# Kernel tuning notes

Measured on AMD Instinct MI355X. Metric: run time of the kernel, lower is better.

Reference implementation:

```python
import jax, jax.numpy as jnp
import numpy as np

B, S, V = 2, 4096, 50265
L, DM, DFF = 2, 768, 3072
H, D, W = 12, 64, 256  # heads, head_dim, one-sided window (attention_window=512)
NEG = -1e9


def _ln(x, s, b, eps=1e-5):
    m = x.mean(-1, keepdims=True)
    v = ((x - m) ** 2).mean(-1, keepdims=True)
    return (x - m) * jax.lax.rsqrt(v + eps) * s + b


def _heads(y):  # [B,S,DM] -> [B,H,S,D]
    return y.reshape(B, S, H, D).transpose(0, 2, 1, 3)


def _longformer_layer(x, am, p):
    nb = S // W  # number of query blocks
    scale = 1.0 / jnp.sqrt(jnp.asarray(D, x.dtype))
    q = _heads(x @ p['Wq'] + p['bq']) * scale
    k = _heads(x @ p['Wk'] + p['bk'])
    v = _heads(x @ p['Wv'] + p['bv'])
    # overlapping key blocks: block n covers padded positions [n*W, n*W+3W)
    idx = jnp.arange(nb)[:, None] * W + jnp.arange(3 * W)[None, :]  # [nb,3W]
    kp = jnp.pad(k, ((0, 0), (0, 0), (W, W), (0, 0)))
    vp = jnp.pad(v, ((0, 0), (0, 0), (W, W), (0, 0)))
    kb = kp[:, :, idx]  # [B,H,nb,3W,D]
    vb = vp[:, :, idx]
    qb = q.reshape(B, H, nb, W, D)
    scores = jnp.einsum('bhnqd,bhnkd->bhnqk', qb, kb)  # [B,H,nb,W,3W]
    # band mask: query i attends keys within +-W
    qi = jnp.arange(W)[:, None]
    kj = jnp.arange(3 * W)[None, :]
    band = (kj >= qi) & (kj <= qi + 2 * W)  # [W,3W]
    kpos = idx - W  # global key positions, [nb,3W]
    valid = (kpos >= 0) & (kpos < S) & (kpos != 0)  # exclude global tok 0 from band
    amk = jnp.pad(am, ((0, 0), (W, W)))[:, idx] > 0  # [B,nb,3W]
    mask = band[None, None, None] & valid[None, None, :, None, :] & amk[:, None, :, None, :]
    scores = jnp.where(mask, scores, NEG).reshape(B, H, S, 3 * W)
    # global-key column: every query attends token 0 (regular K/V)
    sg = jnp.einsum('bhsd,bhd->bhs', q, k[:, :, 0])
    sg = jnp.where(am[:, None, 0:1] > 0, sg, NEG)
    attn = jax.nn.softmax(jnp.concatenate([scores, sg[..., None]], -1), axis=-1)
    a_band = attn[..., :3 * W].reshape(B, H, nb, W, 3 * W)
    out = jnp.einsum('bhnqk,bhnkd->bhnqd', a_band, vb).reshape(B, H, S, D)
    out = out + attn[..., 3 * W][..., None] * v[:, :, 0][:, :, None, :]
    # global query row (token 0): full attention with dedicated global projections
    qg = ((x[:, 0] @ p['Wqg'] + p['bqg']).reshape(B, H, D)) * scale
    kg = _heads(x @ p['Wkg'] + p['bkg'])
    vg = _heads(x @ p['Wvg'] + p['bvg'])
    sgl = jnp.einsum('bhd,bhsd->bhs', qg, kg)
    sgl = jnp.where(am[:, None, :] > 0, sgl, NEG)
    og = jnp.einsum('bhs,bhsd->bhd', jax.nn.softmax(sgl, axis=-1), vg)
    out = out.at[:, :, 0, :].set(og)
    attn_out = out.transpose(0, 2, 1, 3).reshape(B, S, DM) @ p['Wo'] + p['bo']
    x = _ln(x + attn_out, p['ln1_s'], p['ln1_b'])
    h = jax.nn.gelu(x @ p['W1'] + p['b1']) @ p['W2'] + p['b2']
    return _ln(x + h, p['ln2_s'], p['ln2_b'])


def setup_inputs() -> dict:
    key = jax.random.key(0)
    ks = iter(jax.random.split(key, 40))
    f = lambda *s: jax.random.normal(next(ks), s, jnp.float32) * 0.02
    inp = {
        'input_ids': jax.random.randint(next(ks), (B, S), 0, V),
        'attention_mask': jnp.ones((B, S), jnp.int32),
        'word_emb': f(V, DM), 'pos_emb': f(S, DM),
        'ln_e_s': jnp.ones((DM,)), 'ln_e_b': jnp.zeros((DM,)),
        'Wq': f(L, DM, DM), 'bq': jnp.zeros((L, DM)),
        'Wk': f(L, DM, DM), 'bk': jnp.zeros((L, DM)),
        'Wv': f(L, DM, DM), 'bv': jnp.zeros((L, DM)),
        'Wqg': f(L, DM, DM), 'bqg': jnp.zeros((L, DM)),
        'Wkg': f(L, DM, DM), 'bkg': jnp.zeros((L, DM)),
        'Wvg': f(L, DM, DM), 'bvg': jnp.zeros((L, DM)),
        'Wo': f(L, DM, DM), 'bo': jnp.zeros((L, DM)),
        'ln1_s': jnp.ones((L, DM)), 'ln1_b': jnp.zeros((L, DM)),
        'W1': f(L, DM, DFF), 'b1': jnp.zeros((L, DFF)),
        'W2': f(L, DFF, DM), 'b2': jnp.zeros((L, DM)),
        'ln2_s': jnp.ones((L, DM)), 'ln2_b': jnp.zeros((L, DM)),
        'Wcls': f(DM, 2), 'bcls': jnp.zeros((2,)),
    }
    return inp


def reference(input_ids, attention_mask, word_emb, pos_emb, ln_e_s, ln_e_b,
              Wq, bq, Wk, bk, Wv, bv, Wqg, bqg, Wkg, bkg, Wvg, bvg, Wo, bo,
              ln1_s, ln1_b, W1, b1, W2, b2, ln2_s, ln2_b, Wcls, bcls):
    x = word_emb[input_ids] + pos_emb[None]
    x = _ln(x, ln_e_s, ln_e_b)
    for l in range(L):
        p = dict(Wq=Wq[l], bq=bq[l], Wk=Wk[l], bk=bk[l], Wv=Wv[l], bv=bv[l],
                 Wqg=Wqg[l], bqg=bqg[l], Wkg=Wkg[l], bkg=bkg[l], Wvg=Wvg[l], bvg=bvg[l],
                 Wo=Wo[l], bo=bo[l], ln1_s=ln1_s[l], ln1_b=ln1_b[l],
                 W1=W1[l], b1=b1[l], W2=W2[l], b2=b2[l], ln2_s=ln2_s[l], ln2_b=ln2_b[l])
        x = _longformer_layer(x, attention_mask, p)
    return x[:, 0] @ Wcls + bcls  # logits [B, num_labels]
```

## Files before the change

### kernel.cpp

```cpp
#include <hip/hip_runtime.h>
#include <hip/hip_bf16.h>

#define B_   2
#define S_   4096
#define DM_  768
#define H_   12
#define D_   64
#define W_   256
#define NB_  16
#define DFF_ 3072
#define L_   2
#define QS_  3840
#define NEG_ (-1.0e9f)
#define GC_  16

typedef long long ll;
typedef unsigned short u16;
typedef unsigned int   u32;

typedef __attribute__((ext_vector_type(8))) short bfrag;
typedef __attribute__((ext_vector_type(4))) float ffrag;
typedef __attribute__((address_space(1))) unsigned gu32;
typedef __attribute__((address_space(3))) unsigned lu32;

__device__ __forceinline__ float b2f(u16 u){ union{u32 i; float f;} x; x.i = ((u32)u)<<16; return x.f; }
__device__ __forceinline__ u16 f2b(float f){
  __hip_bfloat16 h = __float2bfloat16(f);
  union{__hip_bfloat16 h; u16 u;} x; x.h = h; return x.u;
}
__device__ __forceinline__ void unp8(uint4 u, float* f){
  union{u32 i; float v;} a;
  a.i = u.x<<16; f[0]=a.v; a.i = u.x&0xffff0000u; f[1]=a.v;
  a.i = u.y<<16; f[2]=a.v; a.i = u.y&0xffff0000u; f[3]=a.v;
  a.i = u.z<<16; f[4]=a.v; a.i = u.z&0xffff0000u; f[5]=a.v;
  a.i = u.w<<16; f[6]=a.v; a.i = u.w&0xffff0000u; f[7]=a.v;
}
__device__ __forceinline__ void gld16(const void* g, void* l){
  __builtin_amdgcn_global_load_lds((gu32*)g, (lu32*)l, 16, 0, 0);
}
__device__ __forceinline__ float bsum256(float v, float* s4){
  #pragma unroll
  for(int o=32;o>0;o>>=1) v += __shfl_down(v,o,64);
  int w = threadIdx.x>>6;
  __syncthreads();
  if((threadIdx.x&63)==0) s4[w]=v;
  __syncthreads();
  return s4[0]+s4[1]+s4[2]+s4[3];
}
__device__ __forceinline__ float bmax256(float v, float* s4){
  #pragma unroll
  for(int o=32;o>0;o>>=1) v = fmaxf(v,__shfl_down(v,o,64));
  int w = threadIdx.x>>6;
  __syncthreads();
  if((threadIdx.x&63)==0) s4[w]=v;
  __syncthreads();
  return fmaxf(fmaxf(s4[0],s4[1]),fmaxf(s4[2],s4[3]));
}
__device__ __forceinline__ float gelu_f(float x){
  return 0.5f*x*(1.0f+tanhf(0.7978845608028654f*(x+0.044715f*x*x*x)));
}

__global__ void k_detect(const void* les, int* flag){
  unsigned u = *(const unsigned*)les;
  *flag = (u == 0x3F803F80u) ? 1 : 0;
}

__global__ void k_cvt(const void* __restrict__ src, ll soff, float* __restrict__ dst, int n, const int* flag){
  int f = *flag;
  int i = blockIdx.x*256 + threadIdx.x;
  int st = gridDim.x*256;
  if(f){
    const u16* s = (const u16*)src + soff;
    for(; i<n; i+=st) dst[i] = b2f(s[i]);
  } else {
    const float* s = (const float*)src + soff;
    for(; i<n; i+=st) dst[i] = s[i];
  }
}

struct CvtArgs { const void* src[32]; float* dst[32]; int soff[32]; int n[32]; };
__global__ void k_cvts(CvtArgs a, const int* __restrict__ flag){
  int seg = blockIdx.y;
  int i = blockIdx.x*256 + threadIdx.x;
  if(i >= a.n[seg]) return;
  int f = *flag;
  float v = f ? b2f(((const u16*)a.src[seg])[a.soff[seg]+i])
              : ((const float*)a.src[seg])[a.soff[seg]+i];
  a.dst[seg][i] = v;
}

__global__ __launch_bounds__(256) void k_tw(const void* __restrict__ src, ll soff, u16* __restrict__ dst,
    int R, int C, const int* __restrict__ flag){
  __shared__ float tile[32][33];
  int f = *flag;
  int tx = threadIdx.x & 31, ty = threadIdx.x >> 5;
  int c = blockIdx.x*32 + tx;
  #pragma unroll
  for(int i=0;i<4;i++){
    int r = blockIdx.y*32 + ty + i*8;
    float v;
    if(f) v = b2f(((const u16*)src)[soff + (ll)r*C + c]);
    else  v = ((const float*)src)[soff + (ll)r*C + c];
    tile[ty + i*8][tx] = v;
  }
  __syncthreads();
  #pragma unroll
  for(int i=0;i<4;i++){
    int orow = blockIdx.x*32 + ty + i*8;
    int oc   = blockIdx.y*32 + tx;
    dst[(ll)orow*R + oc] = f2b(tile[tx][ty + i*8]);
  }
}

struct TwArgs { const void* src[14]; ll soff[14]; u16* dst[14]; };
__global__ __launch_bounds__(256) void k_tws(TwArgs a, const int* __restrict__ flag){
  __shared__ float tile[32][33];
  int z = blockIdx.z;
  const void* src = a.src[z]; ll soff = a.soff[z]; u16* dst = a.dst[z];
  int f = *flag;
  int tx = threadIdx.x & 31, ty = threadIdx.x >> 5;
  int c = blockIdx.x*32 + tx;
  #pragma unroll
  for(int i=0;i<4;i++){
    int r = blockIdx.y*32 + ty + i*8;
    float v;
    if(f) v = b2f(((const u16*)src)[soff + (ll)r*DM_ + c]);
    else  v = ((const float*)src)[soff + (ll)r*DM_ + c];
    tile[ty + i*8][tx] = v;
  }
  __syncthreads();
  #pragma unroll
  for(int i=0;i<4;i++){
    int orow = blockIdx.x*32 + ty + i*8;
    int oc   = blockIdx.y*32 + tx;
    dst[(ll)orow*DM_ + oc] = f2b(tile[tx][ty + i*8]);
  }
}

__global__ __launch_bounds__(256) void k_embed(const int* __restrict__ ids, const void* __restrict__ wemb,
    const float* __restrict__ pos, const float* __restrict__ es, const float* __restrict__ eb,
    float* __restrict__ x, u16* __restrict__ xb, const int* flag){
  __shared__ float s4[4];
  int tok = blockIdx.x;
  int s = tok & (S_-1);
  int t = threadIdx.x;
  int id = ids[tok];
  int f = *flag;
  float v[3];
  #pragma unroll
  for(int j=0;j<3;j++){
    int i = t + j*256;
    float we = f ? b2f(((const u16*)wemb)[(ll)id*DM_ + i])
                 : ((const float*)wemb)[(ll)id*DM_ + i];
    v[j] = we + pos[s*DM_ + i];
  }
  float mean = bsum256(v[0]+v[1]+v[2], s4) * (1.0f/DM_);
  float d0=v[0]-mean, d1=v[1]-mean, d2=v[2]-mean;
  float var = bsum256(d0*d0+d1*d1+d2*d2, s4) * (1.0f/DM_);
  float r = rsqrtf(var + 1e-5f);
  #pragma unroll
  for(int j=0;j<3;j++){
    int i = t + j*256;
    float o = (v[j]-mean)*r*es[i] + eb[i];
    x[(ll)tok*DM_ + i] = o;
    xb[(ll)tok*DM_ + i] = f2b(o);
  }
}

__global__ __launch_bounds__(256) void k_rln(float* __restrict__ x, const float* __restrict__ add,
    const float* __restrict__ sc, const float* __restrict__ bi, u16* __restrict__ xb){
  __shared__ float s4[4];
  int tok = blockIdx.x;
  int t = threadIdx.x;
  float v[3];
  #pragma unroll
  for(int j=0;j<3;j++){
    int i = t + j*256;
    v[j] = x[(ll)tok*DM_+i] + add[(ll)tok*DM_+i];
  }
  float mean = bsum256(v[0]+v[1]+v[2], s4) * (1.0f/DM_);
  float d0=v[0]-mean, d1=v[1]-mean, d2=v[2]-mean;
  float var = bsum256(d0*d0+d1*d1+d2*d2, s4) * (1.0f/DM_);
  float r = rsqrtf(var + 1e-5f);
  #pragma unroll
  for(int j=0;j<3;j++){
    int i = t + j*256;
    float o = (v[j]-mean)*r*sc[i] + bi[i];
    x[(ll)tok*DM_+i] = o;
    xb[(ll)tok*DM_+i] = f2b(o);
  }
}

template<int MODE>
__global__ __launch_bounds__(256) void k_mm(const u16* __restrict__ A, const u16* __restrict__ Bt,
    const float* __restrict__ bias, void* __restrict__ Cout, int M, int N, int K){
  __shared__ __align__(16) u16 As[128*32];
  __shared__ __align__(16) u16 Bs[128*32];
  int tid = threadIdx.x, wave = tid>>6, lane = tid&63;
  int m0 = blockIdx.y*128, n0 = blockIdx.x*128;
  int wm = (wave>>1)*64, wn = (wave&1)*64;
  ffrag acc[4][4];
  #pragma unroll
  for(int i=0;i<4;i++)
    #pragma unroll
    for(int j=0;j<4;j++) acc[i][j] = (ffrag){0.f,0.f,0.f,0.f};
  int lrow = lane>>2, lseg = (lane&3)*8;
  const u16* Ap0 = A  + (ll)(m0 + wave*32 + lrow)*K + lseg;
  const u16* Bp0 = Bt + (ll)(n0 + wave*32 + lrow)*K + lseg;
  u16* AsW0 = As + (wave*2+0)*512;
  u16* AsW1 = As + (wave*2+1)*512;
  u16* BsW0 = Bs + (wave*2+0)*512;
  u16* BsW1 = Bs + (wave*2+1)*512;
  int lane15 = lane&15, quad = lane>>4;
  const u16* ArA = As + (wm + lane15)*32 + quad*8;
  const u16* BrB = Bs + (wn + lane15)*32 + quad*8;
  for(int k0=0; k0<K; k0+=32){
    __syncthreads();
    gld16(Ap0 + k0,             AsW0);
    gld16(Ap0 + k0 + (ll)16*K,  AsW1);
    gld16(Bp0 + k0,             BsW0);
    gld16(Bp0 + k0 + (ll)16*K,  BsW1);
    __syncthreads();
    bfrag af[4], bf[4];
    #pragma unroll
    for(int i=0;i<4;i++) af[i] = *(const bfrag*)(ArA + i*512);
    #pragma unroll
    for(int i=0;i<4;i++) bf[i] = *(const bfrag*)(BrB + i*512);
    #pragma unroll
    for(int i=0;i<4;i++)
      #pragma unroll
      for(int j=0;j<4;j++)
        acc[i][j] = __builtin_amdgcn_mfma_f32_16x16x32_bf16(af[i], bf[j], acc[i][j], 0, 0, 0);
  }
  #pragma unroll
  for(int mi=0;mi<4;mi++){
    #pragma unroll
    for(int ni=0;ni<4;ni++){
      int col = n0 + wn + ni*16 + lane15;
      float bv = bias[col];
      #pragma unroll
      for(int r=0;r<4;r++){
        int row = m0 + wm + mi*16 + quad*4 + r;
        float c = acc[mi][ni][r] + bv;
        if(MODE==2) c = gelu_f(c);
        if(MODE==1) ((float*)Cout)[(ll)row*N + col] = c;
        else        ((u16*)Cout)[(ll)row*N + col] = f2b(c);
      }
    }
  }
}

__global__ __launch_bounds__(256) void k_qg(const float* __restrict__ x, const u16* __restrict__ Wt,
    const float* __restrict__ bg, float* __restrict__ qg){
  int b = blockIdx.y;
  int nn = blockIdx.x*256 + threadIdx.x;
  __shared__ float xs[DM_];
  int t = threadIdx.x;
  #pragma unroll
  for(int j=0;j<3;j++) xs[t + j*256] = x[(ll)(b*S_)*DM_ + t + j*256];
  __syncthreads();
  const uint4* wr = (const uint4*)(Wt + (ll)nn*DM_);
  float acc = bg[nn];
  #pragma unroll 4
  for(int g=0; g<96; g++){
    float tf[8]; unp8(wr[g], tf);
    #pragma unroll
    for(int e=0;e<8;e++) acc = fmaf(xs[g*8+e], tf[e], acc);
  }
  qg[b*DM_ + nn] = acc;
}

__global__ __launch_bounds__(256) void k_band(const u16* __restrict__ qb, const u16* __restrict__ kb,
    const u16* __restrict__ vb, const int* __restrict__ am, u16* __restrict__ aout){
  int n = blockIdx.x, h = blockIdx.y, b = blockIdx.z;
  int tid = threadIdx.x;
  int wave = tid>>6, lane = tid&63, lane15 = lane&15, quad = lane>>4;
  int wq = wave*64;
  __shared__ __align__(16) u16 Ks[32*72];
  __shared__ __align__(16) u16 Vt[64*40];
  __shared__ __align__(16) u16 Ps[4][64*40];
  __shared__ float k0f[64];
  __shared__ float v0f[64];
  __shared__ float cok[32];
  const int kbase = n*W_ - W_;
  const int am0 = am[b*S_];
  bfrag aq[4][2];
  {
    const u16* qbase = qb + ((ll)(b*S_ + n*W_ + wq + lane15))*QS_ + h*64 + quad*8;
    #pragma unroll
    for(int mi=0;mi<4;mi++)
      #pragma unroll
      for(int kc=0;kc<2;kc++)
        aq[mi][kc] = *(const bfrag*)(qbase + (ll)mi*16*QS_ + kc*32);
  }
  if(tid < 64){
    k0f[tid] = b2f(kb[(ll)(b*S_)*QS_ + h*64 + tid]);
    v0f[tid] = b2f(vb[(ll)(b*S_)*QS_ + h*64 + tid]);
  }
  ffrag ao[4][4];
  #pragma unroll
  for(int i=0;i<4;i++)
    #pragma unroll
    for(int j=0;j<4;j++) ao[i][j] = (ffrag){0.f,0.f,0.f,0.f};
  float ms[16], ls[16];
  #pragma unroll
  for(int i=0;i<16;i++){ ms[i] = -INFINITY; ls[i] = 0.f; }

  #pragma unroll 1
  for(int c=0;c<24;c++){
    __syncthreads();
    {
      int key = tid>>3, seg = tid&7;
      int kp = kbase + c*32 + key;
      uint4 kvec = make_uint4(0,0,0,0), vvec = make_uint4(0,0,0,0);
      if((unsigned)kp < (unsigned)S_){
        kvec = *(const uint4*)(kb + ((ll)(b*S_+kp))*QS_ + h*64 + seg*8);
        vvec = *(const uint4*)(vb + ((ll)(b*S_+kp))*QS_ + h*64 + seg*8);
      }
      *(uint4*)&Ks[key*72 + seg*8] = kvec;
      u16 vs[8]; *(uint4*)vs = vvec;
      #pragma unroll
      for(int i=0;i<8;i++) Vt[(seg*8+i)*40 + key] = vs[i];
      if(tid < 32){
        int kp2 = kbase + c*32 + tid;
        cok[tid] = ((kp2>=1) && (kp2<S_) && (am[b*S_+kp2]>0)) ? 0.f : NEG_;
      }
    }
    __syncthreads();
    ffrag as_[4][2];
    #pragma unroll
    for(int mi=0;mi<4;mi++)
      #pragma unroll
      for(int ni=0;ni<2;ni++) as_[mi][ni] = (ffrag){0.f,0.f,0.f,0.f};
    #pragma unroll
    for(int ni=0;ni<2;ni++){
      #pragma unroll
      for(int kc=0;kc<2;kc++){
        bfrag bk = *(const bfrag*)&Ks[(ni*16+lane15)*72 + kc*32 + quad*8];
        #pragma unroll
        for(int mi=0;mi<4;mi++)
          as_[mi][ni] = __builtin_amdgcn_mfma_f32_16x16x32_bf16(aq[mi][kc], bk, as_[mi][ni], 0, 0, 0);
      }
    }
    float c0 = cok[lane15], c1 = cok[16+lane15];
    int jg0 = c*32 + lane15, jg1 = jg0 + 16;
    #pragma unroll
    for(int mi=0;mi<4;mi++){
      #pragma unroll
      for(int reg=0;reg<4;reg++){
        int qloc = wq + mi*16 + quad*4 + reg;
        float s0 = ((unsigned)(jg0 - qloc) <= 512u) ? as_[mi][0][reg]*0.125f + c0 : NEG_;
        float s1 = ((unsigned)(jg1 - qloc) <= 512u) ? as_[mi][1][reg]*0.125f + c1 : NEG_;
        float cm = fmaxf(s0, s1);
        cm = fmaxf(cm, __shfl_xor(cm,1));
        cm = fmaxf(cm, __shfl_xor(cm,2));
        cm = fmaxf(cm, __shfl_xor(cm,4));
        cm = fmaxf(cm, __shfl_xor(cm,8));
        int si = mi*4 + reg;
        float mn = fmaxf(ms[si], cm);
        float al = __expf(ms[si] - mn);
        float p0 = __expf(s0 - mn), p1 = __expf(s1 - mn);
        float rs = p0 + p1;
        rs += __shfl_xor(rs,1); rs += __shfl_xor(rs,2);
        rs += __shfl_xor(rs,4); rs += __shfl_xor(rs,8);
        ls[si] = ls[si]*al + rs;
        ms[si] = mn;
        #pragma unroll
        for(int nt=0;nt<4;nt++) ao[mi][nt][reg] *= al;
        int prow = mi*16 + quad*4 + reg;
        Ps[wave][prow*40 + lane15]      = f2b(p0);
        Ps[wave][prow*40 + 16 + lane15] = f2b(p1);
      }
    }
    bfrag bv[4];
    #pragma unroll
    for(int nt=0;nt<4;nt++) bv[nt] = *(const bfrag*)&Vt[(nt*16+lane15)*40 + quad*8];
    #pragma unroll
    for(int mi=0;mi<4;mi++){
      bfrag ap = *(const bfrag*)&Ps[wave][(mi*16+lane15)*40 + quad*8];
      #pragma unroll
      for(int nt=0;nt<4;nt++)
        ao[mi][nt] = __builtin_amdgcn_mfma_f32_16x16x32_bf16(ap, bv[nt], ao[mi][nt], 0, 0, 0);
    }
  }
  float k0v[16];
  #pragma unroll
  for(int kc=0;kc<2;kc++)
    #pragma unroll
    for(int j=0;j<8;j++) k0v[kc*8+j] = k0f[kc*32 + quad*8 + j];
  float cokg = (am0>0) ? 0.f : NEG_;
  float sgm[4];
  #pragma unroll
  for(int mi=0;mi<4;mi++){
    float d = 0.f;
    #pragma unroll
    for(int kc=0;kc<2;kc++)
      #pragma unroll
      for(int j=0;j<8;j++)
        d = fmaf(b2f((u16)aq[mi][kc][j]), k0v[kc*8+j], d);
    d += __shfl_xor(d,16);
    d += __shfl_xor(d,32);
    sgm[mi] = d*0.125f + cokg;
  }
  float v0v[4];
  #pragma unroll
  for(int nt=0;nt<4;nt++) v0v[nt] = v0f[nt*16 + lane15];
  #pragma unroll
  for(int mi=0;mi<4;mi++){
    #pragma unroll
    for(int reg=0;reg<4;reg++){
      int si = mi*4 + reg;
      float sg = __shfl(sgm[mi], (quad<<4) + quad*4 + reg);
      float mn = fmaxf(ms[si], sg);
      float al = __expf(ms[si] - mn);
      float pg = __expf(sg - mn);
      float inv = 1.f / (ls[si]*al + pg);
      #pragma unroll
      for(int nt=0;nt<4;nt++)
        ao[mi][nt][reg] = (ao[mi][nt][reg]*al + pg*v0v[nt]) * inv;
    }
  }
  u16* obase = aout + ((ll)(b*S_ + n*W_ + wq + quad*4))*DM_ + h*64 + lane15;
  #pragma unroll
  for(int mi=0;mi<4;mi++)
    #pragma unroll
    for(int reg=0;reg<4;reg++)
      #pragma unroll
      for(int nt=0;nt<4;nt++)
        obase[(ll)(mi*16+reg)*DM_ + nt*16] = f2b(ao[mi][nt][reg]);
}

__global__ __launch_bounds__(256) void k_gattn1(const float* __restrict__ qg, const u16* __restrict__ kg,
    const u16* __restrict__ vg, const int* __restrict__ am, float* __restrict__ part){
  int ck = blockIdx.x, h = blockIdx.y, b = blockIdx.z;
  int t = threadIdx.x;
  __shared__ float s4[4];
  __shared__ float qgs[64];
  __shared__ float ps[256];
  __shared__ float obuf[4][64];
  if(t < 64) qgs[t] = qg[b*DM_ + h*64 + t];
  __syncthreads();
  int s = ck*256 + t;
  const uint4* kr = (const uint4*)(kg + (ll)(b*S_+s)*QS_ + h*64);
  float d = 0.f;
  #pragma unroll
  for(int g=0; g<8; g++){
    float tf[8]; unp8(kr[g], tf);
    #pragma unroll
    for(int e=0;e<8;e++) d = fmaf(qgs[g*8+e], tf[e], d);
  }
  float sc = (am[b*S_+s] > 0) ? d*0.125f : NEG_;
  float m_c = bmax256(sc, s4);
  float p = __expf(sc - m_c);
  float l_c = bsum256(p, s4);
  ps[t] = p;
  __syncthreads();
  int dd = t & 63, grp = t >> 6;
  float acc = 0.f;
  const u16* vbase = vg + (ll)(b*S_ + ck*256 + grp*64)*QS_ + h*64 + dd;
  #pragma unroll 8
  for(int j=0;j<64;j++)
    acc = fmaf(ps[grp*64+j], b2f(vbase[(ll)j*QS_]), acc);
  obuf[grp][dd] = acc;
  __syncthreads();
  if(t < 64){
    float o = obuf[0][t] + obuf[1][t] + obuf[2][t] + obuf[3][t];
    float* pp = part + ((ll)(b*H_+h)*GC_ + ck)*66;
    if(t == 0){ pp[0] = m_c; pp[1] = l_c; }
    pp[2+t] = o;
  }
}

__global__ void k_gattn2(const float* __restrict__ part, u16* __restrict__ aout){
  int h = blockIdx.x, b = blockIdx.y;
  int t = threadIdx.x;
  const float* pp = part + ((ll)(b*H_+h)*GC_)*66;
  float m = -INFINITY;
  #pragma unroll
  for(int c=0;c<GC_;c++) m = fmaxf(m, pp[c*66]);
  float l = 0.f, o = 0.f;
  #pragma unroll
  for(int c=0;c<GC_;c++){
    float w = __expf(pp[c*66] - m);
    l += pp[c*66+1]*w;
    o += pp[c*66+2+t]*w;
  }
  aout[(ll)(b*S_)*DM_ + h*64 + t] = f2b(o/l);
}

__global__ __launch_bounds__(256) void k_cls(const float* __restrict__ x, const float* __restrict__ Wc,
    const float* __restrict__ bc, void* out, const int* flag){
  __shared__ float s4[4];
  int t = threadIdx.x;
  float a00=0,a01=0,a10=0,a11=0;
  for(int k=t;k<DM_;k+=256){
    float w0 = Wc[k*2], w1 = Wc[k*2+1];
    float x0 = x[k];
    float x1 = x[(ll)S_*DM_ + k];
    a00 = fmaf(x0,w0,a00); a01 = fmaf(x0,w1,a01);
    a10 = fmaf(x1,w0,a10); a11 = fmaf(x1,w1,a11);
  }
  float r00 = bsum256(a00,s4);
  float r01 = bsum256(a01,s4);
  float r10 = bsum256(a10,s4);
  float r11 = bsum256(a11,s4);
  if(t==0){
    float o[4] = {r00+bc[0], r01+bc[1], r10+bc[0], r11+bc[1]};
    if(*flag){
      __hip_bfloat16* ob = (__hip_bfloat16*)out;
      for(int i=0;i<4;i++) ob[i] = __float2bfloat16(o[i]);
    } else {
      float* of = (float*)out;
      for(int i=0;i<4;i++) of[i] = o[i];
    }
  }
}

extern "C" void kernel_launch(void* const* d_in, const int* in_sizes, int n_in,
                              void* d_out, int out_size, void* d_ws, size_t ws_size,
                              hipStream_t stream){
  char* wsb = (char*)d_ws;
  size_t off = 0;
  auto alloc = [&](size_t bytes)->size_t{ off = (off + 255) & ~(size_t)255; size_t r = off; off += bytes; return r; };
  const size_t TOK = (size_t)B_*S_;
  size_t P_flag = alloc(16);
  size_t P_pos  = alloc((size_t)S_*DM_*4);
  size_t P_les  = alloc(DM_*4), P_leb = alloc(DM_*4);
  size_t P_bqkv = alloc((size_t)L_*QS_*4);
  size_t P_bqg  = alloc((size_t)L_*DM_*4);
  size_t P_bo   = alloc((size_t)L_*DM_*4);
  size_t P_b1   = alloc((size_t)L_*DFF_*4);
  size_t P_b2   = alloc((size_t)L_*DM_*4);
  size_t P_l1s  = alloc((size_t)L_*DM_*4), P_l1b = alloc((size_t)L_*DM_*4);
  size_t P_l2s  = alloc((size_t)L_*DM_*4), P_l2b = alloc((size_t)L_*DM_*4);
  size_t P_Wc   = alloc(DM_*2*4), P_bc = alloc(64);
  size_t P_qgb  = alloc((size_t)B_*DM_*4);
  size_t P_part = alloc((size_t)B_*H_*GC_*66*4);
  size_t P_Wqkvt= alloc((size_t)L_*QS_*DM_*2);
  size_t P_Wqgt = alloc((size_t)L_*DM_*DM_*2);
  size_t P_Wot  = alloc((size_t)L_*DM_*DM_*2);
  size_t P_W1t  = alloc((size_t)L_*DM_*DFF_*2);
  size_t P_W2t  = alloc((size_t)L_*DFF_*DM_*2);
  size_t P_x    = alloc(TOK*DM_*4);
  size_t P_tmp  = alloc(TOK*DM_*4);
  size_t P_xb   = alloc(TOK*DM_*2);
  size_t P_qkv  = alloc(TOK*QS_*2);
  size_t P_aout = alloc(TOK*DM_*2);
  size_t P_h    = alloc(TOK*DFF_*2);

  int* flag = (int*)(wsb + P_flag);
  #define FP(o) ((float*)(wsb + (o)))
  #define HP(o) ((u16*)(wsb + (o)))

  k_detect<<<1,1,0,stream>>>(d_in[4], flag);

  k_cvt<<<2048,256,0,stream>>>(d_in[3], 0, FP(P_pos), S_*DM_, flag);

  {
    CvtArgs ca{};
    int ns = 0;
    auto addcv = [&](int idx, size_t dstoff, int soff, int nelem){
      ca.src[ns] = d_in[idx]; ca.dst[ns] = FP(dstoff); ca.soff[ns] = soff; ca.n[ns] = nelem; ns++;
    };
    addcv(4, P_les, 0, DM_); addcv(5, P_leb, 0, DM_);
    addcv(28, P_Wc, 0, DM_*2); addcv(29, P_bc, 0, 2);
    const int bidx[5] = {7,9,11,15,17};
    for(int l=0;l<L_;l++){
      for(int s=0;s<5;s++) addcv(bidx[s], P_bqkv + ((size_t)l*QS_ + s*DM_)*4, l*DM_, DM_);
      addcv(13, P_bqg + (size_t)l*DM_*4,  l*DM_,  DM_);
      addcv(19, P_bo  + (size_t)l*DM_*4,  l*DM_,  DM_);
      addcv(23, P_b1  + (size_t)l*DFF_*4, l*DFF_, DFF_);
      addcv(25, P_b2  + (size_t)l*DM_*4,  l*DM_,  DM_);
      addcv(20, P_l1s + (size_t)l*DM_*4,  l*DM_,  DM_);
      addcv(21, P_l1b + (size_t)l*DM_*4,  l*DM_,  DM_);
      addcv(26, P_l2s + (size_t)l*DM_*4,  l*DM_,  DM_);
      addcv(27, P_l2b + (size_t)l*DM_*4,  l*DM_,  DM_);
    }
    for(int s2=ns; s2<32; s2++){ ca.src[s2]=d_in[4]; ca.dst[s2]=FP(P_les); ca.soff[s2]=0; ca.n[s2]=0; }
    k_cvts<<<dim3(12, ns),256,0,stream>>>(ca, flag);
  }

  {
    TwArgs ta{};
    int nt_ = 0;
    const int widx[5] = {6,8,10,14,16};
    for(int l=0;l<L_;l++){
      for(int s=0;s<5;s++){
        ta.src[nt_] = d_in[widx[s]]; ta.soff[nt_] = (ll)l*DM_*DM_;
        ta.dst[nt_] = HP(P_Wqkvt) + (size_t)l*QS_*DM_ + (size_t)s*DM_*DM_; nt_++;
      }
      ta.src[nt_] = d_in[12]; ta.soff[nt_] = (ll)l*DM_*DM_;
      ta.dst[nt_] = HP(P_Wqgt) + (size_t)l*DM_*DM_; nt_++;
      ta.src[nt_] = d_in[18]; ta.soff[nt_] = (ll)l*DM_*DM_;
      ta.dst[nt_] = HP(P_Wot) + (size_t)l*DM_*DM_; nt_++;
    }
    k_tws<<<dim3(24,24,14),256,0,stream>>>(ta, flag);
  }
  for(int l=0;l<L_;l++){
    k_tw<<<dim3(DFF_/32, DM_/32),256,0,stream>>>(d_in[22], (ll)l*DM_*DFF_,
        HP(P_W1t) + (size_t)l*DFF_*DM_, DM_, DFF_, flag);
    k_tw<<<dim3(DM_/32, DFF_/32),256,0,stream>>>(d_in[24], (ll)l*DFF_*DM_,
        HP(P_W2t) + (size_t)l*DM_*DFF_, DFF_, DM_, flag);
  }

  const int* am = (const int*)d_in[1];
  k_embed<<<(int)TOK,256,0,stream>>>((const int*)d_in[0], d_in[2], FP(P_pos), FP(P_les), FP(P_leb),
                                     FP(P_x), HP(P_xb), flag);
  for(int l=0;l<L_;l++){
    const u16* Wqkvt_l = HP(P_Wqkvt) + (size_t)l*QS_*DM_;
    k_mm<0><<<dim3(QS_/128, TOK/128),256,0,stream>>>(HP(P_xb), Wqkvt_l, FP(P_bqkv) + (size_t)l*QS_,
        HP(P_qkv), (int)TOK, QS_, DM_);
    k_qg<<<dim3(3,B_),256,0,stream>>>(FP(P_x), HP(P_Wqgt) + (size_t)l*DM_*DM_, FP(P_bqg) + (size_t)l*DM_, FP(P_qgb));
    k_band<<<dim3(NB_,H_,B_),256,0,stream>>>(HP(P_qkv), HP(P_qkv)+DM_, HP(P_qkv)+2*DM_, am, HP(P_aout));
    k_gattn1<<<dim3(GC_,H_,B_),256,0,stream>>>(FP(P_qgb), HP(P_qkv)+3*DM_, HP(P_qkv)+4*DM_, am, FP(P_part));
    k_gattn2<<<dim3(H_,B_),64,0,stream>>>(FP(P_part), HP(P_aout));
    k_mm<1><<<dim3(DM_/128, TOK/128),256,0,stream>>>(HP(P_aout), HP(P_Wot) + (size_t)l*DM_*DM_,
        FP(P_bo) + (size_t)l*DM_, FP(P_tmp), (int)TOK, DM_, DM_);
    k_rln<<<(int)TOK,256,0,stream>>>(FP(P_x), FP(P_tmp), FP(P_l1s) + (size_t)l*DM_, FP(P_l1b) + (size_t)l*DM_, HP(P_xb));
    k_mm<2><<<dim3(DFF_/128, TOK/128),256,0,stream>>>(HP(P_xb), HP(P_W1t) + (size_t)l*DFF_*DM_,
        FP(P_b1) + (size_t)l*DFF_, HP(P_h), (int)TOK, DFF_, DM_);
    k_mm<1><<<dim3(DM_/128, TOK/128),256,0,stream>>>(HP(P_h), HP(P_W2t) + (size_t)l*DM_*DFF_,
        FP(P_b2) + (size_t)l*DM_, FP(P_tmp), (int)TOK, DM_, DFF_);
    k_rln<<<(int)TOK,256,0,stream>>>(FP(P_x), FP(P_tmp), FP(P_l2s) + (size_t)l*DM_, FP(P_l2b) + (size_t)l*DM_, HP(P_xb));
  }
  k_cls<<<1,256,0,stream>>>(FP(P_x), FP(P_Wc), FP(P_bc), d_out, flag);
}
```

Before: 1.210 ms.

## Shrink band-attention query tiles to 64 rows and trim key chunks

The band attention kernel now gives each block 64 queries (16 per wave) instead of 256, and the grid grows from 16 to 64 query blocks per head. Each block walks only the 18 key chunks its window can reach rather than 24, which cuts the computation wasted on fully masked keys. The V transpose load is rewritten so each lane gathers a column with scalar loads, and the P tile in shared memory uses XOR swizzling to reduce bank conflicts. The trade-off is that each K/V chunk now feeds only 64 queries, so global K/V traffic per query rises and the scalar V gathers are less coalesced.

```diff
diff --git a/kernel.cpp b/kernel.cpp
--- a/kernel.cpp
+++ b/kernel.cpp
@@ -13,6 +13,8 @@
 #define QS_  3840
 #define NEG_ (-1.0e9f)
 #define GC_  16
+#define QB_  64
+#define NCH_ 18
 
 typedef long long ll;
 typedef unsigned short u16;
@@ -272,116 +274,105 @@
 
 __global__ __launch_bounds__(256) void k_band(const u16* __restrict__ qb, const u16* __restrict__ kb,
     const u16* __restrict__ vb, const int* __restrict__ am, u16* __restrict__ aout){
-  int n = blockIdx.x, h = blockIdx.y, b = blockIdx.z;
+  int nq = blockIdx.x, h = blockIdx.y, b = blockIdx.z;
+  int q0 = nq*QB_;
   int tid = threadIdx.x;
   int wave = tid>>6, lane = tid&63, lane15 = lane&15, quad = lane>>4;
-  int wq = wave*64;
+  int wq = wave*16;
   __shared__ __align__(16) u16 Ks[32*72];
   __shared__ __align__(16) u16 Vt[64*40];
-  __shared__ __align__(16) u16 Ps[4][64*40];
+  __shared__ __align__(16) u16 Ps[4][16*40];
   __shared__ float k0f[64];
   __shared__ float v0f[64];
   __shared__ float cok[32];
-  const int kbase = n*W_ - W_;
+  const int kbase = q0 - W_;
   const int am0 = am[b*S_];
-  bfrag aq[4][2];
+  bfrag aq[2];
   {
-    const u16* qbase = qb + ((ll)(b*S_ + n*W_ + wq + lane15))*QS_ + h*64 + quad*8;
-    #pragma unroll
-    for(int mi=0;mi<4;mi++)
-      #pragma unroll
-      for(int kc=0;kc<2;kc++)
-        aq[mi][kc] = *(const bfrag*)(qbase + (ll)mi*16*QS_ + kc*32);
+    const u16* qbase = qb + ((ll)(b*S_ + q0 + wq + lane15))*QS_ + h*64 + quad*8;
+    aq[0] = *(const bfrag*)(qbase);
+    aq[1] = *(const bfrag*)(qbase + 32);
   }
   if(tid < 64){
     k0f[tid] = b2f(kb[(ll)(b*S_)*QS_ + h*64 + tid]);
     v0f[tid] = b2f(vb[(ll)(b*S_)*QS_ + h*64 + tid]);
   }
-  ffrag ao[4][4];
-  #pragma unroll
-  for(int i=0;i<4;i++)
-    #pragma unroll
-    for(int j=0;j<4;j++) ao[i][j] = (ffrag){0.f,0.f,0.f,0.f};
-  float ms[16], ls[16];
-  #pragma unroll
-  for(int i=0;i<16;i++){ ms[i] = -INFINITY; ls[i] = 0.f; }
+  ffrag ao[4];
+  #pragma unroll
+  for(int j=0;j<4;j++) ao[j] = (ffrag){0.f,0.f,0.f,0.f};
+  float ms[4], ls[4];
+  #pragma unroll
+  for(int i=0;i<4;i++){ ms[i] = -INFINITY; ls[i] = 0.f; }
 
   #pragma unroll 1
-  for(int c=0;c<24;c++){
+  for(int c=0;c<NCH_;c++){
     __syncthreads();
     {
       int key = tid>>3, seg = tid&7;
       int kp = kbase + c*32 + key;
-      uint4 kvec = make_uint4(0,0,0,0), vvec = make_uint4(0,0,0,0);
-      if((unsigned)kp < (unsigned)S_){
+      uint4 kvec = make_uint4(0,0,0,0);
+      if((unsigned)kp < (unsigned)S_)
         kvec = *(const uint4*)(kb + ((ll)(b*S_+kp))*QS_ + h*64 + seg*8);
-        vvec = *(const uint4*)(vb + ((ll)(b*S_+kp))*QS_ + h*64 + seg*8);
+      *(uint4*)&Ks[key*72 + seg*8] = kvec;
+      int kpv = kbase + c*32 + wave*8;
+      union { u16 s[8]; uint4 v; } vu;
+      #pragma unroll
+      for(int j=0;j<8;j++){
+        int kp2 = kpv + j;
+        vu.s[j] = ((unsigned)kp2 < (unsigned)S_) ? vb[((ll)(b*S_+kp2))*QS_ + h*64 + lane] : (u16)0;
       }
-      *(uint4*)&Ks[key*72 + seg*8] = kvec;
-      u16 vs[8]; *(uint4*)vs = vvec;
-      #pragma unroll
-      for(int i=0;i<8;i++) Vt[(seg*8+i)*40 + key] = vs[i];
+      *(uint4*)&Vt[lane*40 + wave*8] = vu.v;
       if(tid < 32){
         int kp2 = kbase + c*32 + tid;
         cok[tid] = ((kp2>=1) && (kp2<S_) && (am[b*S_+kp2]>0)) ? 0.f : NEG_;
       }
     }
     __syncthreads();
-    ffrag as_[4][2];
-    #pragma unroll
-    for(int mi=0;mi<4;mi++)
-      #pragma unroll
-      for(int ni=0;ni<2;ni++) as_[mi][ni] = (ffrag){0.f,0.f,0.f,0.f};
+    ffrag as_[2];
+    as_[0] = (ffrag){0.f,0.f,0.f,0.f};
+    as_[1] = (ffrag){0.f,0.f,0.f,0.f};
     #pragma unroll
     for(int ni=0;ni<2;ni++){
       #pragma unroll
       for(int kc=0;kc<2;kc++){
         bfrag bk = *(const bfrag*)&Ks[(ni*16+lane15)*72 + kc*32 + quad*8];
-        #pragma unroll
-        for(int mi=0;mi<4;mi++)
-          as_[mi][ni] = __builtin_amdgcn_mfma_f32_16x16x32_bf16(aq[mi][kc], bk, as_[mi][ni], 0, 0, 0);
+        as_[ni] = __builtin_amdgcn_mfma_f32_16x16x32_bf16(aq[kc], bk, as_[ni], 0, 0, 0);
       }
     }
     float c0 = cok[lane15], c1 = cok[16+lane15];
     int jg0 = c*32 + lane15, jg1 = jg0 + 16;
     #pragma unroll
-    for(int mi=0;mi<4;mi++){
+    for(int reg=0;reg<4;reg++){
+      int qloc = wq + quad*4 + reg;
+      float s0 = ((unsigned)(jg0 - qloc) <= 512u) ? as_[0][reg]*0.125f + c0 : NEG_;
+      float s1 = ((unsigned)(jg1 - qloc) <= 512u) ? as_[1][reg]*0.125f + c1 : NEG_;
+      float cm = fmaxf(s0, s1);
+      cm = fmaxf(cm, __shfl_xor(cm,1));
+      cm = fmaxf(cm, __shfl_xor(cm,2));
+      cm = fmaxf(cm, __shfl_xor(cm,4));
+      cm = fmaxf(cm, __shfl_xor(cm,8));
+      float mn = fmaxf(ms[reg], cm);
+      float al = __expf(ms[reg] - mn);
+      float p0 = __expf(s0 - mn), p1 = __expf(s1 - mn);
+      float rs = p0 + p1;
+      rs += __shfl_xor(rs,1); rs += __shfl_xor(rs,2);
+      rs += __shfl_xor(rs,4); rs += __shfl_xor(rs,8);
+      ls[reg] = ls[reg]*al + rs;
+      ms[reg] = mn;
       #pragma unroll
-      for(int reg=0;reg<4;reg++){
-        int qloc = wq + mi*16 + quad*4 + reg;
-        float s0 = ((unsigned)(jg0 - qloc) <= 512u) ? as_[mi][0][reg]*0.125f + c0 : NEG_;
-        float s1 = ((unsigned)(jg1 - qloc) <= 512u) ? as_[mi][1][reg]*0.125f + c1 : NEG_;
-        float cm = fmaxf(s0, s1);
-        cm = fmaxf(cm, __shfl_xor(cm,1));
-        cm = fmaxf(cm, __shfl_xor(cm,2));
-        cm = fmaxf(cm, __shfl_xor(cm,4));
-        cm = fmaxf(cm, __shfl_xor(cm,8));
-        int si = mi*4 + reg;
-        float mn = fmaxf(ms[si], cm);
-        float al = __expf(ms[si] - mn);
-        float p0 = __expf(s0 - mn), p1 = __expf(s1 - mn);
-        float rs = p0 + p1;
-        rs += __shfl_xor(rs,1); rs += __shfl_xor(rs,2);
-        rs += __shfl_xor(rs,4); rs += __shfl_xor(rs,8);
-        ls[si] = ls[si]*al + rs;
-        ms[si] = mn;
-        #pragma unroll
-        for(int nt=0;nt<4;nt++) ao[mi][nt][reg] *= al;
-        int prow = mi*16 + quad*4 + reg;
-        Ps[wave][prow*40 + lane15]      = f2b(p0);
-        Ps[wave][prow*40 + 16 + lane15] = f2b(p1);
-      }
+      for(int nt=0;nt<4;nt++) ao[nt][reg] *= al;
+      int prow = quad*4 + reg;
+      Ps[wave][prow*40 + (lane15 ^ (quad*8))]        = f2b(p0);
+      Ps[wave][prow*40 + ((16 + lane15) ^ (quad*8))] = f2b(p1);
     }
     bfrag bv[4];
     #pragma unroll
     for(int nt=0;nt<4;nt++) bv[nt] = *(const bfrag*)&Vt[(nt*16+lane15)*40 + quad*8];
-    #pragma unroll
-    for(int mi=0;mi<4;mi++){
-      bfrag ap = *(const bfrag*)&Ps[wave][(mi*16+lane15)*40 + quad*8];
-      #pragma unroll
-      for(int nt=0;nt<4;nt++)
-        ao[mi][nt] = __builtin_amdgcn_mfma_f32_16x16x32_bf16(ap, bv[nt], ao[mi][nt], 0, 0, 0);
-    }
+    int rperm = ((lane15>>2)&3)*8;
+    bfrag ap = *(const bfrag*)&Ps[wave][lane15*40 + ((quad*8) ^ rperm)];
+    #pragma unroll
+    for(int nt=0;nt<4;nt++)
+      ao[nt] = __builtin_amdgcn_mfma_f32_16x16x32_bf16(ap, bv[nt], ao[nt], 0, 0, 0);
   }
   float k0v[16];
   #pragma unroll
@@ -389,45 +380,38 @@
     #pragma unroll
     for(int j=0;j<8;j++) k0v[kc*8+j] = k0f[kc*32 + quad*8 + j];
   float cokg = (am0>0) ? 0.f : NEG_;
-  float sgm[4];
-  #pragma unroll
-  for(int mi=0;mi<4;mi++){
+  float sgm;
+  {
     float d = 0.f;
     #pragma unroll
     for(int kc=0;kc<2;kc++)
       #pragma unroll
       for(int j=0;j<8;j++)
-        d = fmaf(b2f((u16)aq[mi][kc][j]), k0v[kc*8+j], d);
+        d = fmaf(b2f((u16)aq[kc][j]), k0v[kc*8+j], d);
     d += __shfl_xor(d,16);
     d += __shfl_xor(d,32);
-    sgm[mi] = d*0.125f + cokg;
+    sgm = d*0.125f + cokg;
   }
   float v0v[4];
   #pragma unroll
   for(int nt=0;nt<4;nt++) v0v[nt] = v0f[nt*16 + lane15];
   #pragma unroll
-  for(int mi=0;mi<4;mi++){
-    #pragma unroll
-    for(int reg=0;reg<4;reg++){
-      int si = mi*4 + reg;
-      float sg = __shfl(sgm[mi], (quad<<4) + quad*4 + reg);
-      float mn = fmaxf(ms[si], sg);
-      float al = __expf(ms[si] - mn);
-      float pg = __expf(sg - mn);
-      float inv = 1.f / (ls[si]*al + pg);
-      #pragma unroll
-      for(int nt=0;nt<4;nt++)
-        ao[mi][nt][reg] = (ao[mi][nt][reg]*al + pg*v0v[nt]) * inv;
-    }
-  }
-  u16* obase = aout + ((ll)(b*S_ + n*W_ + wq + quad*4))*DM_ + h*64 + lane15;
-  #pragma unroll
-  for(int mi=0;mi<4;mi++)
-    #pragma unroll
-    for(int reg=0;reg<4;reg++)
-      #pragma unroll
-      for(int nt=0;nt<4;nt++)
-        obase[(ll)(mi*16+reg)*DM_ + nt*16] = f2b(ao[mi][nt][reg]);
+  for(int reg=0;reg<4;reg++){
+    float sg = __shfl(sgm, (quad<<4) + quad*4 + reg);
+    float mn = fmaxf(ms[reg], sg);
+    float al = __expf(ms[reg] - mn);
+    float pg = __expf(sg - mn);
+    float inv = 1.f / (ls[reg]*al + pg);
+    #pragma unroll
+    for(int nt=0;nt<4;nt++)
+      ao[nt][reg] = (ao[nt][reg]*al + pg*v0v[nt]) * inv;
+  }
+  u16* obase = aout + ((ll)(b*S_ + q0 + wq + quad*4))*DM_ + h*64 + lane15;
+  #pragma unroll
+  for(int reg=0;reg<4;reg++)
+    #pragma unroll
+    for(int nt=0;nt<4;nt++)
+      obase[(ll)reg*DM_ + nt*16] = f2b(ao[nt][reg]);
 }
 
 __global__ __launch_bounds__(256) void k_gattn1(const float* __restrict__ qg, const u16* __restrict__ kg,
@@ -611,7 +595,7 @@
     k_mm<0><<<dim3(QS_/128, TOK/128),256,0,stream>>>(HP(P_xb), Wqkvt_l, FP(P_bqkv) + (size_t)l*QS_,
         HP(P_qkv), (int)TOK, QS_, DM_);
     k_qg<<<dim3(3,B_),256,0,stream>>>(FP(P_x), HP(P_Wqgt) + (size_t)l*DM_*DM_, FP(P_bqg) + (size_t)l*DM_, FP(P_qgb));
-    k_band<<<dim3(NB_,H_,B_),256,0,stream>>>(HP(P_qkv), HP(P_qkv)+DM_, HP(P_qkv)+2*DM_, am, HP(P_aout));
+    k_band<<<dim3(S_/QB_,H_,B_),256,0,stream>>>(HP(P_qkv), HP(P_qkv)+DM_, HP(P_qkv)+2*DM_, am, HP(P_aout));
     k_gattn1<<<dim3(GC_,H_,B_),256,0,stream>>>(FP(P_qgb), HP(P_qkv)+3*DM_, HP(P_qkv)+4*DM_, am, FP(P_part));
     k_gattn2<<<dim3(H_,B_),64,0,stream>>>(FP(P_part), HP(P_aout));
     k_mm<1><<<dim3(DM_/128, TOK/128),256,0,stream>>>(HP(P_aout), HP(P_Wot) + (size_t)l*DM_*DM_,
```

Result: faster. 1.140 ms (-5.8%).
